# Kernel optimization log

Measured on AMD Instinct MI355X. Metric: run time of the kernel, lower is better.

Reference implementation:

```python
import jax, jax.numpy as jnp
import numpy as np

N, E, IN_DIM, OUT_DIM, R = 50000, 800000, 128, 128, 8


def setup_inputs() -> dict:
    key = jax.random.key(0)
    k1, k2, k3, k4, k5 = jax.random.split(key, 5)
    x = jax.random.normal(k1, (N, IN_DIM), dtype=jnp.float32)
    edge_index = jax.random.randint(k2, (2, E), 0, N, dtype=jnp.int32)
    edge_type = jax.random.randint(k3, (E,), 0, R, dtype=jnp.int32)
    # Xavier-uniform-ish init for parameters
    lim_w = float(np.sqrt(6.0 / (IN_DIM + OUT_DIM)))
    weight = jax.random.uniform(k4, (R, IN_DIM, OUT_DIM), dtype=jnp.float32, minval=-lim_w, maxval=lim_w)
    self_weight = jax.random.uniform(k5, (IN_DIM, OUT_DIM), dtype=jnp.float32, minval=-lim_w, maxval=lim_w)
    return {"x": x, "weight": weight, "self_weight": self_weight,
            "edge_index": edge_index, "edge_type": edge_type}


def reference(x, weight, self_weight, edge_index, edge_type):
    n = x.shape[0]
    r = weight.shape[0]
    d_out = weight.shape[2]
    src, dst = edge_index[0], edge_index[1]
    # undirected: symmetrize edges (directed=False)
    src_all = jnp.concatenate([src, dst])          # [2E]
    dst_all = jnp.concatenate([dst, src])          # [2E]
    et_all = jnp.concatenate([edge_type, edge_type])  # [2E]
    # transform all nodes by every relation weight once: [R, N, D_out]
    xw = jnp.einsum('ni,rio->rno', x, weight)
    # gather per-edge messages already transformed by their relation's W_r
    msg = xw[et_all, src_all]                      # [2E, D_out]
    # fused (relation, dst) segment id -> per-relation scatter-add
    seg = et_all.astype(jnp.int32) * n + dst_all
    agg = jax.ops.segment_sum(msg, seg, num_segments=r * n).reshape(r, n, d_out)
    deg = jax.ops.segment_sum(jnp.ones_like(seg, dtype=x.dtype), seg,
                              num_segments=r * n).reshape(r, n)
    deg_inv = jnp.where(deg > 0, 1.0 / jnp.maximum(deg, 1.0), jnp.zeros_like(deg))
    out = jnp.sum(agg * deg_inv[..., None], axis=0)  # [N, D_out]
    out = out + x @ self_weight                       # self-loop
    return out
```

## Files before the change

### kernel.cpp

```cpp
#include <hip/hip_runtime.h>

#define NN 50000
#define EE 800000
#define RR 8
#define DD 128
#define SS (NN*RR)
#define TE (2*EE)
#define NB 782
#define NBLK 391
#define NS (NB*NBLK)

typedef __attribute__((ext_vector_type(8))) short bf16x8;
typedef __attribute__((ext_vector_type(4))) float f32x4;

__device__ __forceinline__ unsigned short f2bf(float f){
  unsigned int u = __float_as_uint(f);
  u += 0x7fffu + ((u >> 16) & 1u);
  return (unsigned short)(u >> 16);
}
__device__ __forceinline__ float bf_lo(unsigned int w){ return __uint_as_float(w << 16); }
__device__ __forceinline__ float bf_hi(unsigned int w){ return __uint_as_float(w & 0xffff0000u); }

__device__ __forceinline__ void acc8(float* a, uint4 u){
  a[0] += bf_lo(u.x); a[1] += bf_hi(u.x);
  a[2] += bf_lo(u.y); a[3] += bf_hi(u.y);
  a[4] += bf_lo(u.z); a[5] += bf_hi(u.z);
  a[6] += bf_lo(u.w); a[7] += bf_hi(u.w);
}
__device__ __forceinline__ unsigned int pack2(float a, float b){
  return ((unsigned int)f2bf(b) << 16) | (unsigned int)f2bf(a);
}

__device__ __forceinline__ void dir_edge(const int* ei, const int* et, int j,
                                         int& s, int& d, int& t){
  if (j < EE){ s = ei[j]; d = ei[EE + j]; t = et[j]; }
  else { int jj = j - EE; s = ei[EE + jj]; d = ei[jj]; t = et[jj]; }
}

__global__ __launch_bounds__(256) void k_hist(const int* __restrict__ ei,
                                              const int* __restrict__ et,
                                              int* __restrict__ hist){
  __shared__ int h[NB];
  int tid = threadIdx.x, bid = blockIdx.x;
  for (int i = tid; i < NB; i += 256) h[i] = 0;
  __syncthreads();
  int j0 = bid*4096;
  for (int k = tid; k < 4096; k += 256){
    int j = j0 + k;
    if (j < TE){
      int s, d, t; dir_edge(ei, et, j, s, d, t);
      atomicAdd(&h[d >> 6], 1);
    }
  }
  __syncthreads();
  for (int i = tid; i < NB; i += 256) hist[i*NBLK + bid] = h[i];
}

__global__ __launch_bounds__(256) void k_scan1(int* __restrict__ hist,
                                               int* __restrict__ blksum){
  __shared__ int sd[256];
  int b = blockIdx.x, tid = threadIdx.x;
  int base = b*1024 + tid*4;
  int v0 = (base+0 < NS) ? hist[base+0] : 0;
  int v1 = (base+1 < NS) ? hist[base+1] : 0;
  int v2 = (base+2 < NS) ? hist[base+2] : 0;
  int v3 = (base+3 < NS) ? hist[base+3] : 0;
  int ts = v0+v1+v2+v3;
  sd[tid] = ts; __syncthreads();
  for (int o = 1; o < 256; o <<= 1){
    int t = (tid >= o) ? sd[tid-o] : 0;
    __syncthreads();
    sd[tid] += t;
    __syncthreads();
  }
  int ex = sd[tid] - ts;
  if (base+0 < NS) hist[base+0] = ex; ex += v0;
  if (base+1 < NS) hist[base+1] = ex; ex += v1;
  if (base+2 < NS) hist[base+2] = ex; ex += v2;
  if (base+3 < NS) hist[base+3] = ex;
  if (tid == 255) blksum[b] = sd[255];
}

__global__ __launch_bounds__(512) void k_scan2(int* __restrict__ blksum, int nb){
  __shared__ int sd[512];
  int tid = threadIdx.x;
  int v = (tid < nb) ? blksum[tid] : 0;
  sd[tid] = v; __syncthreads();
  for (int o = 1; o < 512; o <<= 1){
    int t = (tid >= o) ? sd[tid-o] : 0;
    __syncthreads();
    sd[tid] += t;
    __syncthreads();
  }
  if (tid < nb) blksum[tid] = sd[tid] - v;
}

__global__ __launch_bounds__(256) void k_scan3(int* __restrict__ hist,
                                               const int* __restrict__ blksum){
  int i = blockIdx.x*blockDim.x + threadIdx.x;
  if (i < NS) hist[i] += blksum[i >> 10];
}

__global__ __launch_bounds__(256) void k_part(const int* __restrict__ ei,
                                              const int* __restrict__ et,
                                              const int* __restrict__ S,
                                              unsigned int* __restrict__ P){
  __shared__ int cur[NB];
  int tid = threadIdx.x, bid = blockIdx.x;
  for (int i = tid; i < NB; i += 256) cur[i] = S[i*NBLK + bid];
  __syncthreads();
  int j0 = bid*4096;
  for (int k = tid; k < 4096; k += 256){
    int j = j0 + k;
    if (j < TE){
      int s, d, t; dir_edge(ei, et, j, s, d, t);
      int b = d >> 6;
      int p = atomicAdd(&cur[b], 1);
      P[p] = (unsigned int)s | ((unsigned int)(d & 63) << 17)
           | ((unsigned int)t << 23);
    }
  }
}

__global__ __launch_bounds__(256) void k_build(const unsigned int* __restrict__ P,
                                               const int* __restrict__ S,
                                               int* __restrict__ esrc,
                                               int* __restrict__ offs){
  __shared__ int h[512], cu[512], sd[256];
  int tid = threadIdx.x, b = blockIdx.x;
  int pstart = S[b*NBLK];
  int pend   = (b+1 < NB) ? S[(b+1)*NBLK] : TE;
  int ne = pend - pstart;
  h[2*tid] = 0; h[2*tid+1] = 0;
  __syncthreads();
  for (int k = tid; k < ne; k += 256){
    unsigned int u = P[pstart + k];
    int lseg = (int)(((u >> 17) & 63u)*8u + (u >> 23));
    atomicAdd(&h[lseg], 1);
  }
  __syncthreads();
  int v0 = h[2*tid], v1 = h[2*tid+1];
  int ts = v0 + v1;
  sd[tid] = ts; __syncthreads();
  for (int o = 1; o < 256; o <<= 1){
    int t = (tid >= o) ? sd[tid-o] : 0;
    __syncthreads();
    sd[tid] += t;
    __syncthreads();
  }
  int ex = sd[tid] - ts;
  cu[2*tid]   = pstart + ex;
  cu[2*tid+1] = pstart + ex + v0;
  int seg0 = b*512;
  if (seg0 + 2*tid     < SS) offs[seg0 + 2*tid]     = cu[2*tid];
  if (seg0 + 2*tid + 1 < SS) offs[seg0 + 2*tid + 1] = cu[2*tid+1];
  if (b == NB-1 && tid == 0) offs[SS] = TE;
  __syncthreads();
  for (int k = tid; k < ne; k += 256){
    unsigned int u = P[pstart + k];
    int lseg = (int)(((u >> 17) & 63u)*8u + (u >> 23));
    int r = atomicAdd(&cu[lseg], 1);
    esrc[r] = (int)(u & 0x1ffffu);
  }
}

__global__ __launch_bounds__(256) void k_conv(const float* __restrict__ x,
                                              const float* __restrict__ w,
                                              const float* __restrict__ sw,
                                              unsigned short* __restrict__ xb,
                                              unsigned short* __restrict__ wb){
  int i = blockIdx.x*blockDim.x + threadIdx.x;
  const int M1 = NN*DD/4;
  if (i < M1){
    float4 v = ((const float4*)x)[i];
    ushort4 o;
    o.x = f2bf(v.x); o.y = f2bf(v.y); o.z = f2bf(v.z); o.w = f2bf(v.w);
    ((ushort4*)xb)[i] = o;
  } else {
    int j = i - M1;
    if (j < 9*DD*DD){
      int r = j >> 14; int rem = j & 16383; int n = rem >> 7; int k = rem & 127;
      float v = (r < 8) ? w[r*16384 + k*128 + n] : sw[k*128 + n];
      wb[j] = f2bf(v);
    }
  }
}

__global__ __launch_bounds__(256) void k_fused(
    const unsigned short* __restrict__ xb,
    const unsigned short* __restrict__ wb,
    const int* __restrict__ offs,
    const int* __restrict__ esrc,
    float* __restrict__ out)
{
  __shared__ __align__(16) unsigned short Alds[2][32][136];
  const int tid  = threadIdx.x;
  const int wave = tid >> 6, lane = tid & 63;
  const int l15  = lane & 15, quad = lane >> 4;
  const int g    = quad;
  const int gl   = l15;
  const int gbase = g << 4;
  const int rowbase = blockIdx.x * 32;

  f32x4 C[2][2];
  #pragma unroll
  for (int m = 0; m < 2; ++m){ C[m][0] = (f32x4)(0.f); C[m][1] = (f32x4)(0.f); }

  auto gather = [&](int rr, int b){
    int v = 0;
    if (rr < 8 && lane < 16){
      int gdj = rowbase + wave*8 + (lane >> 1);
      if (gdj < NN) v = offs[gdj*8 + rr + (lane & 1)];
    }
    #pragma unroll
    for (int p = 0; p < 2; ++p){
      int rl8  = 2*g + p;
      int rowl = wave*8 + rl8;
      int gd   = rowbase + rowl;
      uint4 u = make_uint4(0u,0u,0u,0u);
      if (rr == 8){
        if (gd < NN) u = *(const uint4*)(xb + (size_t)gd*DD + gl*8);
      } else {
        int off = __shfl(v, 2*rl8);
        int end = __shfl(v, 2*rl8 + 1);
        int cnt = (gd < NN) ? (end - off) : 0;
        float a[8] = {0.f,0.f,0.f,0.f,0.f,0.f,0.f,0.f};
        int idxv = 0;
        if (gl < cnt) idxv = esrc[off + gl];
        int cm = cnt < 16 ? cnt : 16;
        int e = 0;
        for (; e + 4 <= cm; e += 4){
          int s0 = __shfl(idxv, gbase + e + 0);
          int s1 = __shfl(idxv, gbase + e + 1);
          int s2 = __shfl(idxv, gbase + e + 2);
          int s3 = __shfl(idxv, gbase + e + 3);
          uint4 u0 = *(const uint4*)(xb + (size_t)s0*DD + gl*8);
          uint4 u1 = *(const uint4*)(xb + (size_t)s1*DD + gl*8);
          uint4 u2 = *(const uint4*)(xb + (size_t)s2*DD + gl*8);
          uint4 u3 = *(const uint4*)(xb + (size_t)s3*DD + gl*8);
          acc8(a, u0); acc8(a, u1); acc8(a, u2); acc8(a, u3);
        }
        for (; e < cm; ++e){
          int s0 = __shfl(idxv, gbase + e);
          uint4 u0 = *(const uint4*)(xb + (size_t)s0*DD + gl*8);
          acc8(a, u0);
        }
        for (int e2 = 16; e2 < cnt; ++e2){
          int s0 = esrc[off + e2];
          uint4 u0 = *(const uint4*)(xb + (size_t)s0*DD + gl*8);
          acc8(a, u0);
        }
        float sc = (cnt > 0) ? (1.0f / (float)cnt) : 0.f;
        u.x = pack2(a[0]*sc, a[1]*sc);
        u.y = pack2(a[2]*sc, a[3]*sc);
        u.z = pack2(a[4]*sc, a[5]*sc);
        u.w = pack2(a[6]*sc, a[7]*sc);
      }
      *(uint4*)&Alds[b][rowl][gl*8] = u;
    }
  };

  gather(0, 0);
  __syncthreads();

  #pragma unroll 1
  for (int rr = 0; rr < 9; ++rr){
    int b = rr & 1;
    if (rr < 8) gather(rr + 1, b ^ 1);

    const unsigned short* wr = wb + rr * 16384;
    bf16x8 bfrag[2][4];
    #pragma unroll
    for (int nt = 0; nt < 2; ++nt)
      #pragma unroll
      for (int ks = 0; ks < 4; ++ks)
        bfrag[nt][ks] = *(const bf16x8*)(wr + (wave*32 + nt*16 + l15)*128 + ks*32 + quad*8);

    #pragma unroll
    for (int m = 0; m < 2; ++m){
      #pragma unroll
      for (int ks = 0; ks < 4; ++ks){
        bf16x8 af = *(const bf16x8*)&Alds[b][m*16 + l15][ks*32 + quad*8];
        C[m][0] = __builtin_amdgcn_mfma_f32_16x16x32_bf16(af, bfrag[0][ks], C[m][0], 0, 0, 0);
        C[m][1] = __builtin_amdgcn_mfma_f32_16x16x32_bf16(af, bfrag[1][ks], C[m][1], 0, 0, 0);
      }
    }
    __syncthreads();
  }

  #pragma unroll
  for (int m = 0; m < 2; ++m){
    #pragma unroll
    for (int nt = 0; nt < 2; ++nt){
      #pragma unroll
      for (int i = 0; i < 4; ++i){
        int row = m*16 + quad*4 + i;
        int gd  = rowbase + row;
        int col = wave*32 + nt*16 + l15;
        if (gd < NN) out[gd*DD + col] = C[m][nt][i];
      }
    }
  }
}

extern "C" void kernel_launch(void* const* d_in, const int* in_sizes, int n_in,
                              void* d_out, int out_size, void* d_ws, size_t ws_size,
                              hipStream_t stream){
  const float* x  = (const float*)d_in[0];
  const float* w  = (const float*)d_in[1];
  const float* sw = (const float*)d_in[2];
  const int*   ei = (const int*)d_in[3];
  const int*   et = (const int*)d_in[4];
  float* out = (float*)d_out;
  char* ws = (char*)d_ws;

  if (ws_size < (size_t)21100000) return;

  unsigned short* xb = (unsigned short*)(ws + 0);
  int*          hist = (int*)(ws + 0);
  int*        blksum = (int*)(ws + 1223168);
  unsigned int*    P = (unsigned int*)(ws + 1225216);
  int*          esrc = (int*)(ws + 12800000);
  int*          offs = (int*)(ws + 19200000);
  unsigned short* wb = (unsigned short*)(ws + 20800016);

  k_hist <<<NBLK, 256, 0, stream>>>(ei, et, hist);
  k_scan1<<<(NS + 1023)/1024, 256, 0, stream>>>(hist, blksum);
  k_scan2<<<1, 512, 0, stream>>>(blksum, (NS + 1023)/1024);
  k_scan3<<<(NS + 255)/256, 256, 0, stream>>>(hist, blksum);
  k_part <<<NBLK, 256, 0, stream>>>(ei, et, hist, P);
  k_build<<<NB, 256, 0, stream>>>(P, hist, esrc, offs);
  k_conv <<<(NN*DD/4 + 9*DD*DD + 255)/256, 256, 0, stream>>>(x, w, sw, xb, wb);
  k_fused<<<(NN + 31)/32, 256, 0, stream>>>(xb, wb, offs, esrc, out);
}
```

Measured before the change: 258.3 us.

## Gather all relations upfront into wide LDS tile with software-pipelined loads

Restructures the fused kernel so each block first gathers and averages neighbor features for all 8 relations plus the self row into a single 32x1152 LDS tile, then runs the 9 MFMA stages with no intermediate barriers. The gather prefetches all edge indices up front and double-buffers the first four neighbor loads of the next (relation,row) pair while the current pair is accumulated, increasing memory-level parallelism. It also adds a min-blocks-per-SM hint of 2 to launch bounds. The costs are much larger LDS use (~74KB per block) and higher register pressure, which limit occupancy, and gather no longer overlaps with the MFMA work.

```diff
diff --git a/kernel.cpp b/kernel.cpp
--- a/kernel.cpp
+++ b/kernel.cpp
@@ -186,88 +186,134 @@
   }
 }
 
-__global__ __launch_bounds__(256) void k_fused(
+__device__ __forceinline__ void issue4(const unsigned short* __restrict__ xb,
+                                       int idxw, int gb, int gl,
+                                       int ebase, int n, uint4 (&u)[4]){
+  #pragma unroll
+  for (int e = 0; e < 4; ++e){
+    u[e] = make_uint4(0u,0u,0u,0u);
+    if (e < n){
+      int s = __shfl(idxw, gb + ebase + e);
+      u[e] = *(const uint4*)(xb + (size_t)s*DD + gl*8);
+    }
+  }
+}
+
+__global__ __launch_bounds__(256, 2) void k_fused(
     const unsigned short* __restrict__ xb,
     const unsigned short* __restrict__ wb,
     const int* __restrict__ offs,
     const int* __restrict__ esrc,
     float* __restrict__ out)
 {
-  __shared__ __align__(16) unsigned short Alds[2][32][136];
+  __shared__ __align__(16) unsigned short A[32][1160];
   const int tid  = threadIdx.x;
   const int wave = tid >> 6, lane = tid & 63;
   const int l15  = lane & 15, quad = lane >> 4;
-  const int g    = quad;
+  const int gw   = quad;
   const int gl   = l15;
-  const int gbase = g << 4;
+  const int gb   = gw << 4;
   const int rowbase = blockIdx.x * 32;
+  const int rw0 = rowbase + 8*wave;
+
+  #pragma unroll
+  for (int p = 0; p < 2; ++p){
+    int rowl = 8*wave + 2*gw + p;
+    int gd = rowbase + rowl;
+    uint4 u = make_uint4(0u,0u,0u,0u);
+    if (gd < NN) u = *(const uint4*)(xb + (size_t)gd*DD + gl*8);
+    *(uint4*)&A[rowl][8*128 + gl*8] = u;
+  }
+
+  int oidx = rw0*8 + lane;
+  int c0i = (oidx     < SS) ? oidx     : SS;
+  int c1i = (oidx + 1 < SS) ? oidx + 1 : SS;
+  int voff = offs[c0i];
+  int vend = offs[c1i];
+  int vcnt = vend - voff;
+
+  int idxv[16];
+  #pragma unroll
+  for (int i = 0; i < 16; ++i){
+    int off = __shfl(voff, gb + i);
+    int cnt = __shfl(vcnt, gb + i);
+    idxv[i] = (gl < cnt) ? esrc[off + gl] : 0;
+  }
+
+  uint4 U0[2][4], U1[2][4];
+  {
+    int c0 = __shfl(vcnt, gb + 0); c0 = c0 < 4 ? c0 : 4;
+    int c1 = __shfl(vcnt, gb + 1); c1 = c1 < 4 ? c1 : 4;
+    issue4(xb, idxv[0], gb, gl, 0, c0, U0[0]);
+    issue4(xb, idxv[1], gb, gl, 0, c1, U1[0]);
+  }
+
+  #pragma unroll
+  for (int ii = 0; ii < 16; ii += 2){
+    const int cur = (ii >> 1) & 1;
+    const int nxt = cur ^ 1;
+    if (ii + 2 < 16){
+      int c0 = __shfl(vcnt, gb + ii + 2); c0 = c0 < 4 ? c0 : 4;
+      int c1 = __shfl(vcnt, gb + ii + 3); c1 = c1 < 4 ? c1 : 4;
+      issue4(xb, idxv[ii+2], gb, gl, 0, c0, U0[nxt]);
+      issue4(xb, idxv[ii+3], gb, gl, 0, c1, U1[nxt]);
+    }
+    int cnt0 = __shfl(vcnt, gb + ii),     cnt1 = __shfl(vcnt, gb + ii + 1);
+    int off0 = __shfl(voff, gb + ii),     off1 = __shfl(voff, gb + ii + 1);
+    int cm0  = cnt0 < 16 ? cnt0 : 16,     cm1  = cnt1 < 16 ? cnt1 : 16;
+    float a0[8] = {0.f,0.f,0.f,0.f,0.f,0.f,0.f,0.f};
+    float a1[8] = {0.f,0.f,0.f,0.f,0.f,0.f,0.f,0.f};
+    #pragma unroll
+    for (int e = 0; e < 4; ++e){ acc8(a0, U0[cur][e]); acc8(a1, U1[cur][e]); }
+    int e0 = cm0 < 4 ? cm0 : 4, e1 = cm1 < 4 ? cm1 : 4;
+    while (e0 < cm0 || e1 < cm1){
+      int n0 = cm0 - e0; n0 = n0 < 0 ? 0 : (n0 > 4 ? 4 : n0);
+      int n1 = cm1 - e1; n1 = n1 < 0 ? 0 : (n1 > 4 ? 4 : n1);
+      uint4 t0[4], t1[4];
+      issue4(xb, idxv[ii],   gb, gl, e0, n0, t0);
+      issue4(xb, idxv[ii+1], gb, gl, e1, n1, t1);
+      #pragma unroll
+      for (int e = 0; e < 4; ++e){ acc8(a0, t0[e]); acc8(a1, t1[e]); }
+      e0 += n0; e1 += n1;
+    }
+    if (cnt0 > 16){
+      for (int e2 = 16; e2 < cnt0; ++e2){
+        int s = esrc[off0 + e2];
+        uint4 u = *(const uint4*)(xb + (size_t)s*DD + gl*8);
+        acc8(a0, u);
+      }
+    }
+    if (cnt1 > 16){
+      for (int e2 = 16; e2 < cnt1; ++e2){
+        int s = esrc[off1 + e2];
+        uint4 u = *(const uint4*)(xb + (size_t)s*DD + gl*8);
+        acc8(a1, u);
+      }
+    }
+    float s0 = cnt0 > 0 ? 1.0f/(float)cnt0 : 0.f;
+    float s1 = cnt1 > 0 ? 1.0f/(float)cnt1 : 0.f;
+    int rowl = 8*wave + 2*gw + (ii >> 3);
+    uint4 w0, w1;
+    w0.x = pack2(a0[0]*s0, a0[1]*s0);
+    w0.y = pack2(a0[2]*s0, a0[3]*s0);
+    w0.z = pack2(a0[4]*s0, a0[5]*s0);
+    w0.w = pack2(a0[6]*s0, a0[7]*s0);
+    w1.x = pack2(a1[0]*s1, a1[1]*s1);
+    w1.y = pack2(a1[2]*s1, a1[3]*s1);
+    w1.z = pack2(a1[4]*s1, a1[5]*s1);
+    w1.w = pack2(a1[6]*s1, a1[7]*s1);
+    *(uint4*)&A[rowl][((ii    ) & 7)*128 + gl*8] = w0;
+    *(uint4*)&A[rowl][((ii + 1) & 7)*128 + gl*8] = w1;
+  }
+
+  __syncthreads();
 
   f32x4 C[2][2];
   #pragma unroll
   for (int m = 0; m < 2; ++m){ C[m][0] = (f32x4)(0.f); C[m][1] = (f32x4)(0.f); }
 
-  auto gather = [&](int rr, int b){
-    int v = 0;
-    if (rr < 8 && lane < 16){
-      int gdj = rowbase + wave*8 + (lane >> 1);
-      if (gdj < NN) v = offs[gdj*8 + rr + (lane & 1)];
-    }
-    #pragma unroll
-    for (int p = 0; p < 2; ++p){
-      int rl8  = 2*g + p;
-      int rowl = wave*8 + rl8;
-      int gd   = rowbase + rowl;
-      uint4 u = make_uint4(0u,0u,0u,0u);
-      if (rr == 8){
-        if (gd < NN) u = *(const uint4*)(xb + (size_t)gd*DD + gl*8);
-      } else {
-        int off = __shfl(v, 2*rl8);
-        int end = __shfl(v, 2*rl8 + 1);
-        int cnt = (gd < NN) ? (end - off) : 0;
-        float a[8] = {0.f,0.f,0.f,0.f,0.f,0.f,0.f,0.f};
-        int idxv = 0;
-        if (gl < cnt) idxv = esrc[off + gl];
-        int cm = cnt < 16 ? cnt : 16;
-        int e = 0;
-        for (; e + 4 <= cm; e += 4){
-          int s0 = __shfl(idxv, gbase + e + 0);
-          int s1 = __shfl(idxv, gbase + e + 1);
-          int s2 = __shfl(idxv, gbase + e + 2);
-          int s3 = __shfl(idxv, gbase + e + 3);
-          uint4 u0 = *(const uint4*)(xb + (size_t)s0*DD + gl*8);
-          uint4 u1 = *(const uint4*)(xb + (size_t)s1*DD + gl*8);
-          uint4 u2 = *(const uint4*)(xb + (size_t)s2*DD + gl*8);
-          uint4 u3 = *(const uint4*)(xb + (size_t)s3*DD + gl*8);
-          acc8(a, u0); acc8(a, u1); acc8(a, u2); acc8(a, u3);
-        }
-        for (; e < cm; ++e){
-          int s0 = __shfl(idxv, gbase + e);
-          uint4 u0 = *(const uint4*)(xb + (size_t)s0*DD + gl*8);
-          acc8(a, u0);
-        }
-        for (int e2 = 16; e2 < cnt; ++e2){
-          int s0 = esrc[off + e2];
-          uint4 u0 = *(const uint4*)(xb + (size_t)s0*DD + gl*8);
-          acc8(a, u0);
-        }
-        float sc = (cnt > 0) ? (1.0f / (float)cnt) : 0.f;
-        u.x = pack2(a[0]*sc, a[1]*sc);
-        u.y = pack2(a[2]*sc, a[3]*sc);
-        u.z = pack2(a[4]*sc, a[5]*sc);
-        u.w = pack2(a[6]*sc, a[7]*sc);
-      }
-      *(uint4*)&Alds[b][rowl][gl*8] = u;
-    }
-  };
-
-  gather(0, 0);
-  __syncthreads();
-
-  #pragma unroll 1
+  #pragma unroll
   for (int rr = 0; rr < 9; ++rr){
-    int b = rr & 1;
-    if (rr < 8) gather(rr + 1, b ^ 1);
-
     const unsigned short* wr = wb + rr * 16384;
     bf16x8 bfrag[2][4];
     #pragma unroll
@@ -275,17 +321,15 @@
       #pragma unroll
       for (int ks = 0; ks < 4; ++ks)
         bfrag[nt][ks] = *(const bf16x8*)(wr + (wave*32 + nt*16 + l15)*128 + ks*32 + quad*8);
-
     #pragma unroll
     for (int m = 0; m < 2; ++m){
       #pragma unroll
       for (int ks = 0; ks < 4; ++ks){
-        bf16x8 af = *(const bf16x8*)&Alds[b][m*16 + l15][ks*32 + quad*8];
+        bf16x8 af = *(const bf16x8*)&A[m*16 + l15][rr*128 + ks*32 + quad*8];
         C[m][0] = __builtin_amdgcn_mfma_f32_16x16x32_bf16(af, bfrag[0][ks], C[m][0], 0, 0, 0);
         C[m][1] = __builtin_amdgcn_mfma_f32_16x16x32_bf16(af, bfrag[1][ks], C[m][1], 0, 0, 0);
       }
     }
-    __syncthreads();
   }
 
   #pragma unroll
```

Measured after the change: 279.5 us. 1.08x slower.

## Software-pipeline neighbor gathers with prefetched indices and register-buffered bursts around MFMA

Applied to the files above, without the earlier changes.

Restructures the fused gather+GEMM loop so edge indices are fetched two relations ahead and the first eight neighbor rows are issued into registers before the MFMA block, with accumulation and the LDS write happening after the MFMAs. Offsets are loaded once per wave, the self-row is preloaded up front, and the relation loop is fully unrolled with launch bounds requesting three blocks per SIMD. The aim is to hide gather latency behind matrix math. In exchange it holds many more live registers (the U buffers), which can cause spills or lower occupancy.

```diff
diff --git a/kernel.cpp b/kernel.cpp
--- a/kernel.cpp
+++ b/kernel.cpp
@@ -186,7 +186,7 @@
   }
 }
 
-__global__ __launch_bounds__(256) void k_fused(
+__global__ __launch_bounds__(256, 3) void k_fused(
     const unsigned short* __restrict__ xb,
     const unsigned short* __restrict__ wb,
     const int* __restrict__ offs,
@@ -199,75 +199,98 @@
   const int l15  = lane & 15, quad = lane >> 4;
   const int g    = quad;
   const int gl   = l15;
-  const int gbase = g << 4;
+  const int lb   = g << 4;
   const int rowbase = blockIdx.x * 32;
+
+  uint4 selfU[2];
+  #pragma unroll
+  for (int p = 0; p < 2; ++p){
+    int gd = rowbase + wave*8 + 2*g + p;
+    selfU[p] = make_uint4(0u,0u,0u,0u);
+    if (gd < NN) selfU[p] = *(const uint4*)(xb + (size_t)gd*DD + gl*8);
+  }
+
+  int sidx = (rowbase + wave*8)*8 + lane;
+  int voff = 0, vcnt = 0;
+  if (sidx < SS){
+    voff = offs[sidx];
+    vcnt = offs[sidx + 1] - voff;
+  }
+
+  int idxbuf[2][2];
+  uint4 U[2][8];
+
+  auto issue_idx = [&](int rq, int bi){
+    #pragma unroll
+    for (int p = 0; p < 2; ++p){
+      int sl  = (2*g + p)*8 + rq;
+      int off = __shfl(voff, sl);
+      int cnt = __shfl(vcnt, sl);
+      idxbuf[bi][p] = 0;
+      if (gl < cnt) idxbuf[bi][p] = esrc[off + gl];
+    }
+  };
+
+  auto issue_bursts = [&](int rq, int bi){
+    #pragma unroll
+    for (int p = 0; p < 2; ++p){
+      int sl  = (2*g + p)*8 + rq;
+      int cnt = __shfl(vcnt, sl);
+      int cm  = cnt < 8 ? cnt : 8;
+      #pragma unroll
+      for (int e = 0; e < 8; ++e){
+        U[p][e] = make_uint4(0u,0u,0u,0u);
+        if (e < cm){
+          int s = __shfl(idxbuf[bi][p], lb + e);
+          U[p][e] = *(const uint4*)(xb + (size_t)s*DD + gl*8);
+        }
+      }
+    }
+  };
+
+  auto finish = [&](int rq, int bi, int lbuf){
+    #pragma unroll
+    for (int p = 0; p < 2; ++p){
+      int sl  = (2*g + p)*8 + rq;
+      int cnt = __shfl(vcnt, sl);
+      int off = __shfl(voff, sl);
+      float a[8] = {0.f,0.f,0.f,0.f,0.f,0.f,0.f,0.f};
+      #pragma unroll
+      for (int e = 0; e < 8; ++e) acc8(a, U[p][e]);
+      int cm16 = cnt < 16 ? cnt : 16;
+      for (int e2 = 8; e2 < cm16; ++e2){
+        int s = __shfl(idxbuf[bi][p], lb + e2);
+        uint4 u = *(const uint4*)(xb + (size_t)s*DD + gl*8);
+        acc8(a, u);
+      }
+      for (int e2 = 16; e2 < cnt; ++e2){
+        int s = esrc[off + e2];
+        uint4 u = *(const uint4*)(xb + (size_t)s*DD + gl*8);
+        acc8(a, u);
+      }
+      float sc = (cnt > 0) ? (1.0f / (float)cnt) : 0.f;
+      uint4 w0;
+      w0.x = pack2(a[0]*sc, a[1]*sc);
+      w0.y = pack2(a[2]*sc, a[3]*sc);
+      w0.z = pack2(a[4]*sc, a[5]*sc);
+      w0.w = pack2(a[6]*sc, a[7]*sc);
+      int rowl = wave*8 + 2*g + p;
+      *(uint4*)&Alds[lbuf][rowl][gl*8] = w0;
+    }
+  };
+
+  issue_idx(0, 0);
+  issue_idx(1, 1);
+  issue_bursts(0, 0);
+  finish(0, 0, 0);
+  __syncthreads();
 
   f32x4 C[2][2];
   #pragma unroll
   for (int m = 0; m < 2; ++m){ C[m][0] = (f32x4)(0.f); C[m][1] = (f32x4)(0.f); }
 
-  auto gather = [&](int rr, int b){
-    int v = 0;
-    if (rr < 8 && lane < 16){
-      int gdj = rowbase + wave*8 + (lane >> 1);
-      if (gdj < NN) v = offs[gdj*8 + rr + (lane & 1)];
-    }
-    #pragma unroll
-    for (int p = 0; p < 2; ++p){
-      int rl8  = 2*g + p;
-      int rowl = wave*8 + rl8;
-      int gd   = rowbase + rowl;
-      uint4 u = make_uint4(0u,0u,0u,0u);
-      if (rr == 8){
-        if (gd < NN) u = *(const uint4*)(xb + (size_t)gd*DD + gl*8);
-      } else {
-        int off = __shfl(v, 2*rl8);
-        int end = __shfl(v, 2*rl8 + 1);
-        int cnt = (gd < NN) ? (end - off) : 0;
-        float a[8] = {0.f,0.f,0.f,0.f,0.f,0.f,0.f,0.f};
-        int idxv = 0;
-        if (gl < cnt) idxv = esrc[off + gl];
-        int cm = cnt < 16 ? cnt : 16;
-        int e = 0;
-        for (; e + 4 <= cm; e += 4){
-          int s0 = __shfl(idxv, gbase + e + 0);
-          int s1 = __shfl(idxv, gbase + e + 1);
-          int s2 = __shfl(idxv, gbase + e + 2);
-          int s3 = __shfl(idxv, gbase + e + 3);
-          uint4 u0 = *(const uint4*)(xb + (size_t)s0*DD + gl*8);
-          uint4 u1 = *(const uint4*)(xb + (size_t)s1*DD + gl*8);
-          uint4 u2 = *(const uint4*)(xb + (size_t)s2*DD + gl*8);
-          uint4 u3 = *(const uint4*)(xb + (size_t)s3*DD + gl*8);
-          acc8(a, u0); acc8(a, u1); acc8(a, u2); acc8(a, u3);
-        }
-        for (; e < cm; ++e){
-          int s0 = __shfl(idxv, gbase + e);
-          uint4 u0 = *(const uint4*)(xb + (size_t)s0*DD + gl*8);
-          acc8(a, u0);
-        }
-        for (int e2 = 16; e2 < cnt; ++e2){
-          int s0 = esrc[off + e2];
-          uint4 u0 = *(const uint4*)(xb + (size_t)s0*DD + gl*8);
-          acc8(a, u0);
-        }
-        float sc = (cnt > 0) ? (1.0f / (float)cnt) : 0.f;
-        u.x = pack2(a[0]*sc, a[1]*sc);
-        u.y = pack2(a[2]*sc, a[3]*sc);
-        u.z = pack2(a[4]*sc, a[5]*sc);
-        u.w = pack2(a[6]*sc, a[7]*sc);
-      }
-      *(uint4*)&Alds[b][rowl][gl*8] = u;
-    }
-  };
-
-  gather(0, 0);
-  __syncthreads();
-
-  #pragma unroll 1
+  #pragma unroll
   for (int rr = 0; rr < 9; ++rr){
-    int b = rr & 1;
-    if (rr < 8) gather(rr + 1, b ^ 1);
-
     const unsigned short* wr = wb + rr * 16384;
     bf16x8 bfrag[2][4];
     #pragma unroll
@@ -276,16 +299,28 @@
       for (int ks = 0; ks < 4; ++ks)
         bfrag[nt][ks] = *(const bf16x8*)(wr + (wave*32 + nt*16 + l15)*128 + ks*32 + quad*8);
 
+    if (rr < 7) issue_bursts(rr + 1, (rr + 1) & 1);
+    if (rr <= 5) issue_idx(rr + 2, rr & 1);
+
     #pragma unroll
     for (int m = 0; m < 2; ++m){
       #pragma unroll
       for (int ks = 0; ks < 4; ++ks){
-        bf16x8 af = *(const bf16x8*)&Alds[b][m*16 + l15][ks*32 + quad*8];
+        bf16x8 af = *(const bf16x8*)&Alds[rr & 1][m*16 + l15][ks*32 + quad*8];
         C[m][0] = __builtin_amdgcn_mfma_f32_16x16x32_bf16(af, bfrag[0][ks], C[m][0], 0, 0, 0);
         C[m][1] = __builtin_amdgcn_mfma_f32_16x16x32_bf16(af, bfrag[1][ks], C[m][1], 0, 0, 0);
       }
     }
-    __syncthreads();
+
+    if (rr < 7) finish(rr + 1, (rr + 1) & 1, (rr + 1) & 1);
+    if (rr == 7){
+      #pragma unroll
+      for (int p = 0; p < 2; ++p){
+        int rowl = wave*8 + 2*g + p;
+        *(uint4*)&Alds[0][rowl][gl*8] = selfU[p];
+      }
+    }
+    if (rr < 8) __syncthreads();
   }
 
   #pragma unroll
```

Measured after the change: 257.6 us. No clear change (-0.3%).

## Aggregate neighbors via MFMA over gathered rows with async global-to-LDS pipeline

Applied to the files above, without the earlier changes.

The fused kernel no longer sums neighbor features with scalar adds. It gathers individual neighbor rows straight into swizzled LDS using global_load_lds in a 4-slot pipeline, then multiplies each gathered slot by W_r with MFMA, accumulating per relation and scaling by 1/deg afterward. Each wave now owns 16 rows and all 128 output columns, the block covers 64 rows, and a zero padding row is appended to xb for masked edges. The matrix work grows by about the maximum degree per relation group, and the per-wave bfrag[8][4] register footprint is large, which trades extra compute and register pressure for overlapped latency and no VALU reduction.

```diff
diff --git a/kernel.cpp b/kernel.cpp
--- a/kernel.cpp
+++ b/kernel.cpp
@@ -17,18 +17,6 @@
   unsigned int u = __float_as_uint(f);
   u += 0x7fffu + ((u >> 16) & 1u);
   return (unsigned short)(u >> 16);
-}
-__device__ __forceinline__ float bf_lo(unsigned int w){ return __uint_as_float(w << 16); }
-__device__ __forceinline__ float bf_hi(unsigned int w){ return __uint_as_float(w & 0xffff0000u); }
-
-__device__ __forceinline__ void acc8(float* a, uint4 u){
-  a[0] += bf_lo(u.x); a[1] += bf_hi(u.x);
-  a[2] += bf_lo(u.y); a[3] += bf_hi(u.y);
-  a[4] += bf_lo(u.z); a[5] += bf_hi(u.z);
-  a[6] += bf_lo(u.w); a[7] += bf_hi(u.w);
-}
-__device__ __forceinline__ unsigned int pack2(float a, float b){
-  return ((unsigned int)f2bf(b) << 16) | (unsigned int)f2bf(a);
 }
 
 __device__ __forceinline__ void dir_edge(const int* ei, const int* et, int j,
@@ -182,123 +170,206 @@
       int r = j >> 14; int rem = j & 16383; int n = rem >> 7; int k = rem & 127;
       float v = (r < 8) ? w[r*16384 + k*128 + n] : sw[k*128 + n];
       wb[j] = f2bf(v);
-    }
-  }
-}
-
-__global__ __launch_bounds__(256) void k_fused(
+    } else if (j < 9*DD*DD + 32){
+      ushort4 z; z.x = 0; z.y = 0; z.z = 0; z.w = 0;
+      ((ushort4*)(xb + (size_t)NN*DD))[j - 9*DD*DD] = z;
+    }
+  }
+}
+
+#define WAITV(n) do { \
+    asm volatile("s_waitcnt vmcnt(" #n ")" ::: "memory"); \
+    __builtin_amdgcn_sched_barrier(0); \
+  } while (0)
+
+__global__ __launch_bounds__(256, 2) void k_fused(
     const unsigned short* __restrict__ xb,
     const unsigned short* __restrict__ wb,
     const int* __restrict__ offs,
     const int* __restrict__ esrc,
     float* __restrict__ out)
 {
-  __shared__ __align__(16) unsigned short Alds[2][32][136];
+  __shared__ __align__(16) unsigned short A[4][4][2048];
   const int tid  = threadIdx.x;
   const int wave = tid >> 6, lane = tid & 63;
   const int l15  = lane & 15, quad = lane >> 4;
-  const int g    = quad;
-  const int gl   = l15;
-  const int gbase = g << 4;
-  const int rowbase = blockIdx.x * 32;
-
-  f32x4 C[2][2];
+  const int srow = lane >> 4;
+  const int scol = lane & 15;
+  const int row0 = blockIdx.x * 64 + wave * 16;
+
+  int voff0 = 0, vcnt0 = 0, voff1 = 0, vcnt1 = 0;
+  {
+    int s0 = row0 * 8 + lane;
+    if (s0 < SS){ voff0 = offs[s0]; vcnt0 = offs[s0 + 1] - voff0; }
+    int s1 = (row0 + 8) * 8 + lane;
+    if (s1 < SS){ voff1 = offs[s1]; vcnt1 = offs[s1 + 1] - voff1; }
+  }
+  float icnt0 = (vcnt0 > 0) ? 1.0f / (float)vcnt0 : 0.0f;
+  float icnt1 = (vcnt1 > 0) ? 1.0f / (float)vcnt1 : 0.0f;
+
+  int redm;
+  {
+    int r0 = vcnt0, r1 = vcnt1;
+    r0 = max(r0, __shfl_xor(r0, 8));  r1 = max(r1, __shfl_xor(r1, 8));
+    r0 = max(r0, __shfl_xor(r0, 16)); r1 = max(r1, __shfl_xor(r1, 16));
+    r0 = max(r0, __shfl_xor(r0, 32)); r1 = max(r1, __shfl_xor(r1, 32));
+    redm = max(r0, r1);
+  }
+
+  f32x4 Ct[8];
   #pragma unroll
-  for (int m = 0; m < 2; ++m){ C[m][0] = (f32x4)(0.f); C[m][1] = (f32x4)(0.f); }
-
-  auto gather = [&](int rr, int b){
-    int v = 0;
-    if (rr < 8 && lane < 16){
-      int gdj = rowbase + wave*8 + (lane >> 1);
-      if (gdj < NN) v = offs[gdj*8 + rr + (lane & 1)];
-    }
-    #pragma unroll
-    for (int p = 0; p < 2; ++p){
-      int rl8  = 2*g + p;
-      int rowl = wave*8 + rl8;
-      int gd   = rowbase + rowl;
-      uint4 u = make_uint4(0u,0u,0u,0u);
-      if (rr == 8){
-        if (gd < NN) u = *(const uint4*)(xb + (size_t)gd*DD + gl*8);
-      } else {
-        int off = __shfl(v, 2*rl8);
-        int end = __shfl(v, 2*rl8 + 1);
-        int cnt = (gd < NN) ? (end - off) : 0;
-        float a[8] = {0.f,0.f,0.f,0.f,0.f,0.f,0.f,0.f};
-        int idxv = 0;
-        if (gl < cnt) idxv = esrc[off + gl];
-        int cm = cnt < 16 ? cnt : 16;
-        int e = 0;
-        for (; e + 4 <= cm; e += 4){
-          int s0 = __shfl(idxv, gbase + e + 0);
-          int s1 = __shfl(idxv, gbase + e + 1);
-          int s2 = __shfl(idxv, gbase + e + 2);
-          int s3 = __shfl(idxv, gbase + e + 3);
-          uint4 u0 = *(const uint4*)(xb + (size_t)s0*DD + gl*8);
-          uint4 u1 = *(const uint4*)(xb + (size_t)s1*DD + gl*8);
-          uint4 u2 = *(const uint4*)(xb + (size_t)s2*DD + gl*8);
-          uint4 u3 = *(const uint4*)(xb + (size_t)s3*DD + gl*8);
-          acc8(a, u0); acc8(a, u1); acc8(a, u2); acc8(a, u3);
-        }
-        for (; e < cm; ++e){
-          int s0 = __shfl(idxv, gbase + e);
-          uint4 u0 = *(const uint4*)(xb + (size_t)s0*DD + gl*8);
-          acc8(a, u0);
-        }
-        for (int e2 = 16; e2 < cnt; ++e2){
-          int s0 = esrc[off + e2];
-          uint4 u0 = *(const uint4*)(xb + (size_t)s0*DD + gl*8);
-          acc8(a, u0);
-        }
-        float sc = (cnt > 0) ? (1.0f / (float)cnt) : 0.f;
-        u.x = pack2(a[0]*sc, a[1]*sc);
-        u.y = pack2(a[2]*sc, a[3]*sc);
-        u.z = pack2(a[4]*sc, a[5]*sc);
-        u.w = pack2(a[6]*sc, a[7]*sc);
+  for (int nt = 0; nt < 8; ++nt) Ct[nt] = (f32x4)(0.f);
+
+  auto stage = [&](int slot, int kk, int idreg){
+    char* lbase = (char*)&A[wave][slot][0];
+    #pragma unroll
+    for (int j = 0; j < 4; ++j){
+      int m  = 4 * j + srow;
+      int id = __shfl(idreg, (m << 2) | (kk & 3));
+      int cs = scol ^ (m & 7);
+      const unsigned short* gp = xb + (size_t)id * DD + cs * 8;
+      __builtin_amdgcn_global_load_lds(
+          (const __attribute__((address_space(1))) void*)gp,
+          (__attribute__((address_space(3))) void*)(lbase + j * 1024),
+          16, 0, 0);
+    }
+  };
+
+  #pragma unroll 1
+  for (int r = 0; r < 8; ++r){
+    int idbuf[4];
+    {
+      int m    = lane >> 2;
+      int srcl = ((m & 7) << 3) | r;
+      int oA = __shfl(voff0, srcl), oB = __shfl(voff1, srcl);
+      int cA = __shfl(vcnt0, srcl), cB = __shfl(vcnt1, srcl);
+      int off = (lane < 32) ? oA : oB;
+      int cnt = (lane < 32) ? cA : cB;
+      #pragma unroll
+      for (int c = 0; c < 4; ++c){
+        int sl = (lane & 3) + 4 * c;
+        idbuf[c] = (sl < cnt) ? esrc[off + sl] : NN;
       }
-      *(uint4*)&Alds[b][rowl][gl*8] = u;
-    }
-  };
-
-  gather(0, 0);
-  __syncthreads();
-
-  #pragma unroll 1
-  for (int rr = 0; rr < 9; ++rr){
-    int b = rr & 1;
-    if (rr < 8) gather(rr + 1, b ^ 1);
-
-    const unsigned short* wr = wb + rr * 16384;
-    bf16x8 bfrag[2][4];
-    #pragma unroll
-    for (int nt = 0; nt < 2; ++nt)
+    }
+
+    const unsigned short* wr = wb + r * 16384;
+    bf16x8 bfrag[8][4];
+    #pragma unroll
+    for (int nt = 0; nt < 8; ++nt)
       #pragma unroll
       for (int ks = 0; ks < 4; ++ks)
-        bfrag[nt][ks] = *(const bf16x8*)(wr + (wave*32 + nt*16 + l15)*128 + ks*32 + quad*8);
-
-    #pragma unroll
-    for (int m = 0; m < 2; ++m){
+        bfrag[nt][ks] = *(const bf16x8*)(wr + (nt*16 + l15)*128 + ks*32 + quad*8);
+
+    int L = __shfl(redm, r);
+
+    if (L > 0) stage(0, 0, idbuf[0]);
+    if (L > 1) stage(1, 1, idbuf[0]);
+    if (L > 2) stage(2, 2, idbuf[0]);
+
+    f32x4 Cr[8];
+    #pragma unroll
+    for (int nt = 0; nt < 8; ++nt) Cr[nt] = (f32x4)(0.f);
+
+    #pragma unroll
+    for (int k = 0; k < 16; ++k){
+      if (k < L){
+        if (k + 3 <= L)      { WAITV(8); }
+        else if (k + 2 == L) { WAITV(4); }
+        else                 { WAITV(0); }
+        if (k + 3 < L) stage((k + 3) & 3, k + 3, idbuf[(k + 3) >> 2]);
+        const char* abase = (const char*)&A[wave][k & 3][0];
+        #pragma unroll
+        for (int ks = 0; ks < 4; ++ks){
+          int cb = ((ks * 32 + quad * 8) * 2) ^ ((l15 & 7) << 4);
+          bf16x8 af = *(const bf16x8*)(abase + l15 * 256 + cb);
+          #pragma unroll
+          for (int nt = 0; nt < 8; ++nt)
+            Cr[nt] = __builtin_amdgcn_mfma_f32_16x16x32_bf16(af, bfrag[nt][ks], Cr[nt], 0, 0, 0);
+        }
+      }
+    }
+
+    if (L > 16){
+      for (int k = 16; k < L; ++k){
+        #pragma unroll
+        for (int j = 0; j < 4; ++j){
+          int m    = 4 * j + srow;
+          int srcl = ((m & 7) << 3) | r;
+          int oA = __shfl(voff0, srcl), oB = __shfl(voff1, srcl);
+          int cA = __shfl(vcnt0, srcl), cB = __shfl(vcnt1, srcl);
+          int off = (j < 2) ? oA : oB;
+          int cnt = (j < 2) ? cA : cB;
+          int id  = (k < cnt) ? esrc[off + k] : NN;
+          int cs  = scol ^ (m & 7);
+          const unsigned short* gp = xb + (size_t)id * DD + cs * 8;
+          __builtin_amdgcn_global_load_lds(
+              (const __attribute__((address_space(1))) void*)gp,
+              (__attribute__((address_space(3))) void*)((char*)&A[wave][0][0] + j * 1024),
+              16, 0, 0);
+        }
+        WAITV(0);
+        const char* abase = (const char*)&A[wave][0][0];
+        #pragma unroll
+        for (int ks = 0; ks < 4; ++ks){
+          int cb = ((ks * 32 + quad * 8) * 2) ^ ((l15 & 7) << 4);
+          bf16x8 af = *(const bf16x8*)(abase + l15 * 256 + cb);
+          #pragma unroll
+          for (int nt = 0; nt < 8; ++nt)
+            Cr[nt] = __builtin_amdgcn_mfma_f32_16x16x32_bf16(af, bfrag[nt][ks], Cr[nt], 0, 0, 0);
+        }
+      }
+    }
+
+    #pragma unroll
+    for (int i = 0; i < 4; ++i){
+      int srcl = ((((quad & 1) * 4) + i) << 3) | r;
+      float sA = __shfl(icnt0, srcl);
+      float sB = __shfl(icnt1, srcl);
+      float s  = (quad < 2) ? sA : sB;
       #pragma unroll
-      for (int ks = 0; ks < 4; ++ks){
-        bf16x8 af = *(const bf16x8*)&Alds[b][m*16 + l15][ks*32 + quad*8];
-        C[m][0] = __builtin_amdgcn_mfma_f32_16x16x32_bf16(af, bfrag[0][ks], C[m][0], 0, 0, 0);
-        C[m][1] = __builtin_amdgcn_mfma_f32_16x16x32_bf16(af, bfrag[1][ks], C[m][1], 0, 0, 0);
-      }
-    }
-    __syncthreads();
+      for (int nt = 0; nt < 8; ++nt)
+        Ct[nt][i] += s * Cr[nt][i];
+    }
+  }
+
+  {
+    const unsigned short* wr = wb + 8 * 16384;
+    bf16x8 bfrag[8][4];
+    #pragma unroll
+    for (int nt = 0; nt < 8; ++nt)
+      #pragma unroll
+      for (int ks = 0; ks < 4; ++ks)
+        bfrag[nt][ks] = *(const bf16x8*)(wr + (nt*16 + l15)*128 + ks*32 + quad*8);
+    #pragma unroll
+    for (int j = 0; j < 4; ++j){
+      int m  = 4 * j + srow;
+      int gd = row0 + m;
+      int id = (gd < NN) ? gd : NN;
+      int cs = scol ^ (m & 7);
+      const unsigned short* gp = xb + (size_t)id * DD + cs * 8;
+      __builtin_amdgcn_global_load_lds(
+          (const __attribute__((address_space(1))) void*)gp,
+          (__attribute__((address_space(3))) void*)((char*)&A[wave][0][0] + j * 1024),
+          16, 0, 0);
+    }
+    WAITV(0);
+    const char* abase = (const char*)&A[wave][0][0];
+    #pragma unroll
+    for (int ks = 0; ks < 4; ++ks){
+      int cb = ((ks * 32 + quad * 8) * 2) ^ ((l15 & 7) << 4);
+      bf16x8 af = *(const bf16x8*)(abase + l15 * 256 + cb);
+      #pragma unroll
+      for (int nt = 0; nt < 8; ++nt)
+        Ct[nt] = __builtin_amdgcn_mfma_f32_16x16x32_bf16(af, bfrag[nt][ks], Ct[nt], 0, 0, 0);
+    }
   }
 
   #pragma unroll
-  for (int m = 0; m < 2; ++m){
-    #pragma unroll
-    for (int nt = 0; nt < 2; ++nt){
-      #pragma unroll
-      for (int i = 0; i < 4; ++i){
-        int row = m*16 + quad*4 + i;
-        int gd  = rowbase + row;
-        int col = wave*32 + nt*16 + l15;
-        if (gd < NN) out[gd*DD + col] = C[m][nt][i];
-      }
+  for (int nt = 0; nt < 8; ++nt){
+    #pragma unroll
+    for (int i = 0; i < 4; ++i){
+      int gr = row0 + quad * 4 + i;
+      if (gr < NN) out[(size_t)gr * DD + nt * 16 + l15] = Ct[nt][i];
     }
   }
 }
@@ -320,9 +391,9 @@
   int*          hist = (int*)(ws + 0);
   int*        blksum = (int*)(ws + 1223168);
   unsigned int*    P = (unsigned int*)(ws + 1225216);
-  int*          esrc = (int*)(ws + 12800000);
-  int*          offs = (int*)(ws + 19200000);
-  unsigned short* wb = (unsigned short*)(ws + 20800016);
+  int*          esrc = (int*)(ws + 12800256);
+  int*          offs = (int*)(ws + 19200256);
+  unsigned short* wb = (unsigned short*)(ws + 20800272);
 
   k_hist <<<NBLK, 256, 0, stream>>>(ei, et, hist);
   k_scan1<<<(NS + 1023)/1024, 256, 0, stream>>>(hist, blksum);
@@ -330,6 +401,6 @@
   k_scan3<<<(NS + 255)/256, 256, 0, stream>>>(hist, blksum);
   k_part <<<NBLK, 256, 0, stream>>>(ei, et, hist, P);
   k_build<<<NB, 256, 0, stream>>>(P, hist, esrc, offs);
-  k_conv <<<(NN*DD/4 + 9*DD*DD + 255)/256, 256, 0, stream>>>(x, w, sw, xb, wb);
-  k_fused<<<(NN + 31)/32, 256, 0, stream>>>(xb, wb, offs, esrc, out);
-}
+  k_conv <<<(NN*DD/4 + 9*DD*DD + 32 + 255)/256, 256, 0, stream>>>(x, w, sw, xb, wb);
+  k_fused<<<(NN + 63)/64, 256, 0, stream>>>(xb, wb, offs, esrc, out);
+}
```

After: 393.9 us. +52.5%, slower.
